# Performance work log

Measured on AMD Instinct MI355X. Metric: run time of the kernel, lower is better.

The kernel has to match this reference:

```python
import jax, jax.numpy as jnp
import numpy as np
from jax import lax

STRIDES = [4, 8, 16, 32, 64]
SIZES = [32.0, 64.0, 128.0, 256.0, 512.0]
RATIOS = [0.5, 1.0, 2.0]
IMG_H = IMG_W = 1024.0
NMS_T = 0.7
PRE = 1000      # PRE_NMS_TOPK_TEST
POST = 1000     # POST_NMS_TOPK_TEST
MIN_SIZE = 0.0
N = 2
FEAT = [(256, 256), (128, 128), (64, 64), (32, 32), (16, 16)]
SCALE_CLAMP = float(np.log(1000.0 / 16.0))


def make_anchors(H, W, stride, size):
    # detectron2 DefaultAnchorGenerator: area=size^2, w=sqrt(area/r), h=w*r; grid offsets = stride*arange
    r = np.array(RATIOS)
    ws = np.sqrt(size * size / r)
    hs = ws * r
    base = np.stack([-ws / 2, -hs / 2, ws / 2, hs / 2], axis=1)  # [A,4]
    sx = np.arange(W) * stride
    sy = np.arange(H) * stride
    yy, xx = np.meshgrid(sy, sx, indexing='ij')
    shifts = np.stack([xx, yy, xx, yy], axis=-1).reshape(-1, 1, 4)  # [H*W,1,4]
    return jnp.asarray((shifts + base[None]).reshape(-1, 4), jnp.float32)  # [H*W*A,4]


def conv2d(x, w, b, pad):
    y = lax.conv_general_dilated(x, w, (1, 1), [(pad, pad), (pad, pad)],
                                 dimension_numbers=('NCHW', 'OIHW', 'NCHW'))
    return y + b[None, :, None, None]


def apply_deltas(deltas, anchors):
    # Box2BoxTransform.apply_deltas with weights (1,1,1,1)
    w = anchors[..., 2] - anchors[..., 0]
    h = anchors[..., 3] - anchors[..., 1]
    cx = anchors[..., 0] + 0.5 * w
    cy = anchors[..., 1] + 0.5 * h
    dx, dy, dw, dh = deltas[..., 0], deltas[..., 1], deltas[..., 2], deltas[..., 3]
    dw = jnp.minimum(dw, SCALE_CLAMP)
    dh = jnp.minimum(dh, SCALE_CLAMP)
    pcx = dx * w + cx
    pcy = dy * h + cy
    pw = jnp.exp(dw) * w
    ph = jnp.exp(dh) * h
    return jnp.stack([pcx - 0.5 * pw, pcy - 0.5 * ph, pcx + 0.5 * pw, pcy + 0.5 * ph], axis=-1)


def pairwise_iou(b):
    area = (b[:, 2] - b[:, 0]) * (b[:, 3] - b[:, 1])
    lt = jnp.maximum(b[:, None, :2], b[None, :, :2])
    rb = jnp.minimum(b[:, None, 2:], b[None, :, 2:])
    wh = jnp.clip(rb - lt, 0.0)
    inter = wh[..., 0] * wh[..., 1]
    return inter / jnp.maximum(area[:, None] + area[None, :] - inter, 1e-9)


def nms_keep(boxes, valid):
    # boxes already sorted by score desc; sequential greedy NMS keep mask
    K = boxes.shape[0]
    M = pairwise_iou(boxes)
    idx = jnp.arange(K)

    def body(i, keep):
        sup = (M[i] > NMS_T) & (idx > i) & keep[i]
        return keep & (~sup)

    return lax.fori_loop(0, K, body, valid)


def rpn_forward(feats, conv_w, conv_b, obj_w, obj_b, delta_w, delta_b):
    all_boxes, all_scores = [], []
    lim = jnp.array([IMG_W, IMG_H, IMG_W, IMG_H], jnp.float32)
    for x, (H, W), stride, size in zip(feats, FEAT, STRIDES, SIZES):
        t = jax.nn.relu(conv2d(x, conv_w, conv_b, 1))
        logits = conv2d(t, obj_w, obj_b, 0)      # [N,A,H,W]
        deltas = conv2d(t, delta_w, delta_b, 0)  # [N,4A,H,W]
        A = logits.shape[1]
        logits = logits.transpose(0, 2, 3, 1).reshape(N, -1)                       # [N,H*W*A]
        deltas = deltas.reshape(N, A, 4, H, W).transpose(0, 3, 4, 1, 2).reshape(N, -1, 4)
        anchors = make_anchors(H, W, stride, size)
        props = apply_deltas(deltas, anchors[None])                                # [N,H*W*A,4]
        k = min(PRE, props.shape[1])
        scores, idx = lax.top_k(logits, k)                                         # [N,k]
        boxes = jnp.take_along_axis(props, idx[..., None], axis=1)                 # [N,k,4]
        boxes = jnp.clip(boxes, 0.0, lim)                                          # clip to image
        valid = ((boxes[..., 2] - boxes[..., 0]) > MIN_SIZE) & ((boxes[..., 3] - boxes[..., 1]) > MIN_SIZE)
        keep = lax.stop_gradient(jax.vmap(nms_keep)(boxes, valid))                 # NMS is no_grad in torch
        all_boxes.append(boxes)
        all_scores.append(jnp.where(keep, scores, -1e9))
    boxes = jnp.concatenate(all_boxes, axis=1)
    scores = jnp.concatenate(all_scores, axis=1)
    fs, fi = lax.top_k(scores, POST)                                               # final sort-by-score
    fb = jnp.take_along_axis(boxes, fi[..., None], axis=1)
    return fb, fs


def setup_inputs() -> dict:
    key = jax.random.key(0)
    ks = jax.random.split(key, 8)
    d = {}
    for i, (name, (H, W)) in enumerate(zip(['p2', 'p3', 'p4', 'p5', 'p6'], FEAT)):
        d[name] = jax.random.normal(ks[i], (N, 256, H, W), jnp.float32)
    d['conv_w'] = jax.random.normal(ks[5], (256, 256, 3, 3), jnp.float32) * 0.01
    d['conv_b'] = jnp.zeros((256,), jnp.float32)
    d['obj_w'] = jax.random.normal(ks[6], (3, 256, 1, 1), jnp.float32) * 0.01
    d['obj_b'] = jnp.zeros((3,), jnp.float32)
    d['delta_w'] = jax.random.normal(ks[7], (12, 256, 1, 1), jnp.float32) * 0.01
    d['delta_b'] = jnp.zeros((12,), jnp.float32)
    return d


def reference(p2, p3, p4, p5, p6, conv_w, conv_b, obj_w, obj_b, delta_w, delta_b):
    return rpn_forward([p2, p3, p4, p5, p6], conv_w, conv_b, obj_w, obj_b, delta_w, delta_b)
```

## Files before the change

kernel.cpp:

```cpp
#include <hip/hip_runtime.h>
#include <stdint.h>

#define DEVI __device__ __forceinline__

#define S_TOT 261888
#define NIMG  2
#define SCLD  4.135166556742356

__constant__ int    c_S[5]    = {196608, 49152, 12288, 3072, 768};
__constant__ int    c_loff[5] = {0, 196608, 245760, 258048, 261120};
__constant__ int    c_K[5]    = {1000, 1000, 1000, 1000, 768};
__constant__ int    c_Wl[5]   = {256, 128, 64, 32, 16};
__constant__ int    c_str[5]  = {4, 8, 16, 32, 64};
__constant__ double c_sz[5]   = {32.0, 64.0, 128.0, 256.0, 512.0};
__constant__ double c_rat[3]  = {0.5, 1.0, 2.0};
__constant__ int    c_boff[6] = {0, 512, 640, 672, 680, 682};
__constant__ int    c_Hl[5]   = {256, 128, 64, 32, 16};

DEVI unsigned key_of(float f) {
  unsigned u = __float_as_uint(f);
  return (u & 0x80000000u) ? ~u : (u | 0x80000000u);
}
DEVI float key_dec(unsigned k) {
  unsigned u = (k & 0x80000000u) ? (k & 0x7fffffffu) : ~k;
  return __uint_as_float(u);
}

__global__ void transpose_w(const float* __restrict__ w, float* __restrict__ wT2) {
  int k  = blockIdx.x;
  int co = threadIdx.x;
  int ci = k / 9, j = k - ci * 9;
  wT2[((size_t)(ci * 8 + (co >> 5))) * 288 + j * 32 + (co & 31)] = w[co * 2304 + k];
}

__global__ __launch_bounds__(512, 4) void conv_fused(
    const float* __restrict__ x0, const float* __restrict__ x1,
    const float* __restrict__ x2, const float* __restrict__ x3,
    const float* __restrict__ x4,
    const float* __restrict__ wT2,
    const float* __restrict__ cb, const float* __restrict__ ow,
    const float* __restrict__ ob, const float* __restrict__ dwt,
    const float* __restrict__ db, float* __restrict__ logits,
    float* __restrict__ deltas)
{
  __shared__ float lds[7680];
  const int tid = threadIdx.x;
  const int n = blockIdx.y;
  const int b = blockIdx.x;
  int l = 0;
#pragma unroll
  for (int q = 1; q < 5; ++q) if (b >= c_boff[q]) l = q;
  const int t = b - c_boff[l];
  const int H = c_Hl[l], W = H;
  const int tx = t & ((16 >> l) - 1), ty = t >> (4 - l);
  const int px0 = tx << 4, py0t = ty << 3;
  const int loff = c_loff[l];
  const float* xin = (l == 0) ? x0 : (l == 1) ? x1 : (l == 2) ? x2 : (l == 3) ? x3 : x4;
  xin += (size_t)n * 256 * H * W;

  const int lane = tid & 63, wv = tid >> 6;
  const int px = lane & 15, py = lane >> 4;
  const int cob = __builtin_amdgcn_readfirstlane(wv);
  const int co0 = cob << 5;

  float a0[32], a1[32];
#pragma unroll
  for (int i = 0; i < 32; ++i) { a0[i] = 0.f; a1[i] = 0.f; }

  for (int ch = 0; ch < 8; ++ch) {
    const int ci0 = ch << 5;
    __syncthreads();
    for (int tt = tid; tt < 32 * 180; tt += 512) {
      int ci = tt / 180, rem = tt % 180;
      int ry = rem / 18, rx = rem % 18;
      int gy = py0t + ry - 1, gx = px0 + rx - 1;
      float v = 0.f;
      if (gy >= 0 && gy < H && gx >= 0 && gx < W)
        v = xin[((size_t)(ci0 + ci) * H + gy) * W + gx];
      lds[tt] = v;
    }
    __syncthreads();
#pragma unroll 1
    for (int cc = 0; cc < 32; ++cc) {
      const int pb = cc * 180 + py * 18 + px;
      float pv0[9], pv1[9];
#pragma unroll
      for (int ky = 0; ky < 3; ++ky)
#pragma unroll
        for (int kx = 0; kx < 3; ++kx) {
          pv0[ky * 3 + kx] = lds[pb + ky * 18 + kx];
          pv1[ky * 3 + kx] = lds[pb + (ky + 4) * 18 + kx];
        }
      const float* wr = wT2 + ((size_t)((ci0 + cc) * 8 + cob)) * 288;
#pragma unroll
      for (int j = 0; j < 9; ++j) {
#pragma unroll
        for (int i = 0; i < 32; ++i) {
          const float wgt = wr[j * 32 + i];
          a0[i] = fmaf(wgt, pv0[j], a0[i]);
          a1[i] = fmaf(wgt, pv1[j], a1[i]);
        }
      }
    }
  }

#pragma unroll
  for (int h = 0; h < 2; ++h) {
    float part[15];
#pragma unroll
    for (int f = 0; f < 15; ++f) part[f] = 0.f;
#pragma unroll
    for (int i = 0; i < 32; ++i) {
      float v = (h ? a1[i] : a0[i]) + cb[co0 + i];
      float tv = fmaxf(v, 0.f);
#pragma unroll
      for (int f = 0; f < 3; ++f)  part[f]     = fmaf(tv, ow[f * 256 + co0 + i],  part[f]);
#pragma unroll
      for (int f = 0; f < 12; ++f) part[3 + f] = fmaf(tv, dwt[f * 256 + co0 + i], part[3 + f]);
    }
    __syncthreads();
#pragma unroll
    for (int f = 0; f < 15; ++f) lds[wv * 960 + f * 64 + lane] = part[f];
    __syncthreads();
    for (int tt = tid; tt < 960; tt += 512) {
      float s = 0.f;
#pragma unroll
      for (int w2 = 0; w2 < 8; ++w2) s += lds[w2 * 960 + tt];
      int f = tt >> 6, p = tt & 63;
      int gx = px0 + (p & 15), gy = py0t + (p >> 4) + 4 * h;
      int cell = gy * W + gx;
      if (f < 3) {
        logits[(size_t)n * S_TOT + loff + cell * 3 + f] = s + ob[f];
      } else {
        int chn = f - 3, a = chn >> 2, c = chn & 3;
        deltas[(((size_t)n * S_TOT + loff + cell * 3 + a) << 2) + c] = s + db[chn];
      }
    }
  }
}

__global__ __launch_bounds__(1024) void topk_kernel(
    const float* __restrict__ logits, const float* __restrict__ deltas,
    float* __restrict__ selscore, float* __restrict__ selbox,
    unsigned* __restrict__ selvalid)
{
  const int tid = threadIdx.x;
  const int nl = blockIdx.x, n = nl / 5, l = nl % 5;
  const int Sl = c_S[l], loff = c_loff[l], Kl = c_K[l], Wl = c_Wl[l], strl = c_str[l];
  const float* sc = logits + (size_t)n * S_TOT + loff;

  __shared__ unsigned hist[256];
  __shared__ unsigned sh_prefix, sh_need, s_base, s_cb;
  __shared__ unsigned waveTot[16], waveOff[16];
  __shared__ unsigned long long sortbuf[1024];

  unsigned prefix = 0, need = (unsigned)Kl;
  for (int p = 0; p < 4; ++p) {
    for (int i = tid; i < 256; i += 1024) hist[i] = 0;
    __syncthreads();
    const int shift = 24 - p * 8;
    for (int i = tid; i < Sl; i += 1024) {
      unsigned k = key_of(sc[i]);
      if (p == 0 || (k >> (shift + 8)) == prefix)
        atomicAdd(&hist[(k >> shift) & 255u], 1u);
    }
    __syncthreads();
    if (tid == 0) {
      unsigned cum = 0;
      for (int b = 255; b >= 0; --b) {
        unsigned c = hist[b];
        if (cum + c >= need) { sh_prefix = (prefix << 8) | (unsigned)b; sh_need = need - cum; break; }
        cum += c;
      }
    }
    __syncthreads();
    prefix = sh_prefix; need = sh_need;
    __syncthreads();
  }
  const unsigned Tkey = prefix;

  if (tid == 0) s_base = 0;
  __syncthreads();
  for (int pass = 0; pass < 2; ++pass) {
    for (int st = 0; st < Sl; st += 1024) {
      const int i = st + tid;
      bool flag = false; unsigned k = 0;
      if (i < Sl) {
        k = key_of(sc[i]);
        flag = (pass == 0) ? (k > Tkey) : (k == Tkey);
      }
      unsigned long long m = __ballot(flag);
      const int lane = tid & 63, w = tid >> 6;
      unsigned mypre = (unsigned)__popcll(m & ((1ull << lane) - 1ull));
      if (lane == 0) waveTot[w] = (unsigned)__popcll(m);
      __syncthreads();
      if (tid == 0) {
        unsigned ss = 0;
        for (int q = 0; q < 16; ++q) { waveOff[q] = ss; ss += waveTot[q]; }
        s_cb = s_base; s_base += ss;
      }
      __syncthreads();
      if (flag) {
        unsigned pos = s_cb + waveOff[w] + mypre;
        if (pos < (unsigned)Kl)
          sortbuf[pos] = (((unsigned long long)k) << 32) |
                         (unsigned long long)(0xFFFFFFFFu - (unsigned)i);
      }
      __syncthreads();
    }
  }
  if (tid >= Kl) sortbuf[tid] = (unsigned long long)(0xFFFFFFFFu - (unsigned)tid);
  __syncthreads();

  for (int k2 = 2; k2 <= 1024; k2 <<= 1) {
    for (int j = k2 >> 1; j > 0; j >>= 1) {
      const int i = tid, ixj = i ^ j;
      if (ixj > i) {
        unsigned long long a = sortbuf[i], b = sortbuf[ixj];
        const bool desc = (i & k2) == 0;
        if (desc ? (a < b) : (a > b)) { sortbuf[i] = b; sortbuf[ixj] = a; }
      }
      __syncthreads();
    }
  }

  const int r = tid;
  const int o = nl * 1024 + r;
  if (r < Kl) {
    unsigned long long v = sortbuf[r];
    unsigned k = (unsigned)(v >> 32);
    unsigned ai = 0xFFFFFFFFu - (unsigned)(v & 0xFFFFFFFFull);
    float score = key_dec(k);
    int cell = (int)(ai / 3u), a = (int)(ai % 3u);
    int xg = cell % Wl, yg = cell / Wl;
    double rr = c_rat[a], sz = c_sz[l];
    double wsd = sqrt(sz * sz / rr);
    double hw = 0.5 * wsd, hh = 0.5 * wsd * rr;
    double xs = (double)(xg * strl), ys = (double)(yg * strl);
    float a0 = (float)(xs - hw), a1 = (float)(ys - hh);
    float a2 = (float)(xs + hw), a3 = (float)(ys + hh);
    const float* dp = deltas + (((size_t)n * S_TOT + loff + ai) << 2);
    float dx = dp[0], dy = dp[1], dw_ = dp[2], dh_ = dp[3];
    float aw = a2 - a0, ah = a3 - a1;
    float cx = a0 + 0.5f * aw, cy = a1 + 0.5f * ah;
    dw_ = fminf(dw_, (float)SCLD); dh_ = fminf(dh_, (float)SCLD);
    float pcx = dx * aw + cx, pcy = dy * ah + cy;
    float pw = expf(dw_) * aw, ph = expf(dh_) * ah;
    float b0 = fminf(fmaxf(pcx - 0.5f * pw, 0.f), 1024.f);
    float b1 = fminf(fmaxf(pcy - 0.5f * ph, 0.f), 1024.f);
    float b2 = fminf(fmaxf(pcx + 0.5f * pw, 0.f), 1024.f);
    float b3 = fminf(fmaxf(pcy + 0.5f * ph, 0.f), 1024.f);
    unsigned valid = ((b2 - b0) > 0.f && (b3 - b1) > 0.f) ? 1u : 0u;
    selscore[o] = score;
    selbox[o * 4 + 0] = b0; selbox[o * 4 + 1] = b1;
    selbox[o * 4 + 2] = b2; selbox[o * 4 + 3] = b3;
    selvalid[o] = valid;
  } else {
    selscore[o] = -1e9f;
    selbox[o * 4 + 0] = 0.f; selbox[o * 4 + 1] = 0.f;
    selbox[o * 4 + 2] = 0.f; selbox[o * 4 + 3] = 0.f;
    selvalid[o] = 0u;
  }
}

__global__ __launch_bounds__(256) void nms_sup(
    const float* __restrict__ selbox, unsigned long long* __restrict__ sup)
{
  int gid = blockIdx.x * 256 + threadIdx.x;
  int w = gid & 15, i = (gid >> 4) & 1023, nl = gid >> 14;
  if (nl >= 10) return;
  int l = nl % 5, Kl = c_K[l];
  unsigned long long bits = 0;
  if (i < Kl) {
    const float* bi = selbox + (size_t)(nl * 1024 + i) * 4;
    float x0 = bi[0], y0 = bi[1], x1 = bi[2], y1 = bi[3];
    float ar = (x1 - x0) * (y1 - y0);
    int jlo = w * 64; if (jlo < i + 1) jlo = i + 1;
    int jhi = w * 64 + 64; if (jhi > Kl) jhi = Kl;
    for (int j = jlo; j < jhi; ++j) {
      const float* bj = selbox + (size_t)(nl * 1024 + j) * 4;
      float u0 = fmaxf(x0, bj[0]), v0 = fmaxf(y0, bj[1]);
      float u1 = fminf(x1, bj[2]), v1 = fminf(y1, bj[3]);
      float iw = fmaxf(u1 - u0, 0.f), ih = fmaxf(v1 - v0, 0.f);
      float inter = iw * ih;
      float aj = (bj[2] - bj[0]) * (bj[3] - bj[1]);
      float iou = inter / fmaxf(ar + aj - inter, 1e-9f);
      if (iou > 0.7f) bits |= 1ull << (j - w * 64);
    }
  }
  sup[(size_t)(nl * 1024 + i) * 16 + w] = bits;
}

__global__ __launch_bounds__(64) void nms_reduce(
    const unsigned* __restrict__ selvalid, const unsigned long long* __restrict__ sup,
    const float* __restrict__ selscore, float* __restrict__ scnms)
{
  const int nl = blockIdx.x, tid = threadIdx.x;
  const int l = nl % 5, Kl = c_K[l];
  unsigned long long keep = 0;
  if (tid < 16) {
    for (int t = 0; t < 64; ++t) {
      int r = tid * 64 + t;
      if (r < Kl && selvalid[nl * 1024 + r]) keep |= 1ull << t;
    }
  }
  const unsigned long long* srow = sup + (size_t)nl * 1024 * 16;
  unsigned long long rowA = (tid < 16) ? srow[(size_t)0 * 16 + tid] : 0;
  unsigned long long rowB = (tid < 16 && Kl > 1) ? srow[(size_t)1 * 16 + tid] : 0;
  for (int i = 0; i < Kl; i += 2) {
    unsigned long long kw = __shfl(keep, i >> 6);
    unsigned long long cur = rowA;
    rowA = (tid < 16 && i + 2 < Kl) ? srow[(size_t)(i + 2) * 16 + tid] : 0;
    if (((kw >> (i & 63)) & 1ull) && tid < 16) keep &= ~cur;
    kw = __shfl(keep, (i + 1) >> 6);
    cur = rowB;
    rowB = (tid < 16 && i + 3 < Kl) ? srow[(size_t)(i + 3) * 16 + tid] : 0;
    if (((kw >> ((i + 1) & 63)) & 1ull) && tid < 16) keep &= ~cur;
  }
  for (int r = tid; r < 1024; r += 64) {
    unsigned long long wv = __shfl(keep, r >> 6);
    bool kp = (r < Kl) && ((wv >> (r & 63)) & 1ull);
    scnms[nl * 1024 + r] = kp ? selscore[nl * 1024 + r] : -1e9f;
  }
}

DEVI float cand_score(const float* scnms, int n, int g) {
  int l = g / 1000;
  int r = g - l * 1000;
  return scnms[((n * 5 + l) << 10) + r];
}

__global__ __launch_bounds__(1024) void final_topk(
    const float* __restrict__ scnms, const float* __restrict__ selbox,
    float* __restrict__ out)
{
  const int tid = threadIdx.x;
  const int n = blockIdx.x;
  const int S = 4768;

  __shared__ unsigned hist[256];
  __shared__ unsigned sh_prefix, sh_need, s_base, s_cb;
  __shared__ unsigned waveTot[16], waveOff[16];
  __shared__ unsigned long long sortbuf[1024];

  unsigned prefix = 0, need = 1000;
  for (int p = 0; p < 4; ++p) {
    for (int i = tid; i < 256; i += 1024) hist[i] = 0;
    __syncthreads();
    const int shift = 24 - p * 8;
    for (int i = tid; i < S; i += 1024) {
      unsigned k = key_of(cand_score(scnms, n, i));
      if (p == 0 || (k >> (shift + 8)) == prefix)
        atomicAdd(&hist[(k >> shift) & 255u], 1u);
    }
    __syncthreads();
    if (tid == 0) {
      unsigned cum = 0;
      for (int b = 255; b >= 0; --b) {
        unsigned c = hist[b];
        if (cum + c >= need) { sh_prefix = (prefix << 8) | (unsigned)b; sh_need = need - cum; break; }
        cum += c;
      }
    }
    __syncthreads();
    prefix = sh_prefix; need = sh_need;
    __syncthreads();
  }
  const unsigned Tkey = prefix;

  if (tid == 0) s_base = 0;
  __syncthreads();
  for (int pass = 0; pass < 2; ++pass) {
    for (int st = 0; st < S; st += 1024) {
      const int i = st + tid;
      bool flag = false; unsigned k = 0;
      if (i < S) {
        k = key_of(cand_score(scnms, n, i));
        flag = (pass == 0) ? (k > Tkey) : (k == Tkey);
      }
      unsigned long long m = __ballot(flag);
      const int lane = tid & 63, w = tid >> 6;
      unsigned mypre = (unsigned)__popcll(m & ((1ull << lane) - 1ull));
      if (lane == 0) waveTot[w] = (unsigned)__popcll(m);
      __syncthreads();
      if (tid == 0) {
        unsigned ss = 0;
        for (int q = 0; q < 16; ++q) { waveOff[q] = ss; ss += waveTot[q]; }
        s_cb = s_base; s_base += ss;
      }
      __syncthreads();
      if (flag) {
        unsigned pos = s_cb + waveOff[w] + mypre;
        if (pos < 1000u)
          sortbuf[pos] = (((unsigned long long)k) << 32) |
                         (unsigned long long)(0xFFFFFFFFu - (unsigned)i);
      }
      __syncthreads();
    }
  }
  if (tid >= 1000) sortbuf[tid] = (unsigned long long)(0xFFFFFFFFu - (unsigned)tid);
  __syncthreads();

  for (int k2 = 2; k2 <= 1024; k2 <<= 1) {
    for (int j = k2 >> 1; j > 0; j >>= 1) {
      const int i = tid, ixj = i ^ j;
      if (ixj > i) {
        unsigned long long a = sortbuf[i], b = sortbuf[ixj];
        const bool desc = (i & k2) == 0;
        if (desc ? (a < b) : (a > b)) { sortbuf[i] = b; sortbuf[ixj] = a; }
      }
      __syncthreads();
    }
  }

  if (tid < 1000) {
    unsigned long long v = sortbuf[tid];
    unsigned k = (unsigned)(v >> 32);
    int g = (int)(0xFFFFFFFFu - (unsigned)(v & 0xFFFFFFFFull));
    int l = g / 1000, r = g - l * 1000;
    const float* b = selbox + ((size_t)((n * 5 + l) * 1024 + r)) * 4;
    size_t ob_ = ((size_t)n * 1000 + tid) * 4;
    out[ob_ + 0] = b[0]; out[ob_ + 1] = b[1];
    out[ob_ + 2] = b[2]; out[ob_ + 3] = b[3];
    out[8000 + n * 1000 + tid] = key_dec(k);
  }
}

extern "C" void kernel_launch(void* const* d_in, const int* in_sizes, int n_in,
                              void* d_out, int out_size, void* d_ws, size_t ws_size,
                              hipStream_t stream)
{
  const float* feats[5];
  for (int i = 0; i < 5; ++i) feats[i] = (const float*)d_in[i];
  const float* conv_w  = (const float*)d_in[5];
  const float* conv_b  = (const float*)d_in[6];
  const float* obj_w   = (const float*)d_in[7];
  const float* obj_b   = (const float*)d_in[8];
  const float* delta_w = (const float*)d_in[9];
  const float* delta_b = (const float*)d_in[10];

  char* wsp = (char*)d_ws;
  float* wT2      = (float*)wsp;  wsp += (size_t)2304 * 256 * 4;
  float* logits   = (float*)wsp;  wsp += (size_t)NIMG * S_TOT * 4;
  float* deltas   = (float*)wsp;  wsp += (size_t)NIMG * S_TOT * 16;
  float* selscore = (float*)wsp;  wsp += (size_t)10 * 1024 * 4;
  float* selbox   = (float*)wsp;  wsp += (size_t)10 * 1024 * 16;
  unsigned* selvalid = (unsigned*)wsp; wsp += (size_t)10 * 1024 * 4;
  float* scnms    = (float*)wsp;  wsp += (size_t)10 * 1024 * 4;
  unsigned long long* sup = (unsigned long long*)wsp;
  wsp += (size_t)10 * 1024 * 16 * 8;

  transpose_w<<<dim3(2304), dim3(256), 0, stream>>>(conv_w, wT2);

  conv_fused<<<dim3(682, NIMG), dim3(512), 0, stream>>>(
      feats[0], feats[1], feats[2], feats[3], feats[4],
      wT2, conv_b, obj_w, obj_b, delta_w, delta_b, logits, deltas);

  topk_kernel<<<dim3(10), dim3(1024), 0, stream>>>(logits, deltas,
                                                   selscore, selbox, selvalid);
  nms_sup<<<dim3(640), dim3(256), 0, stream>>>(selbox, sup);
  nms_reduce<<<dim3(10), dim3(64), 0, stream>>>(selvalid, sup, selscore, scnms);
  final_topk<<<dim3(NIMG), dim3(1024), 0, stream>>>(scnms, selbox, (float*)d_out);
}
```

Measured before the change: 3.504 ms.

## Retile conv to 16x16 pixel tiles with 16-channel groups in two passes

The fused 3x3 conv now covers a 16x16 pixel tile per block instead of 16x8, which halves the block count. Each wave computes 16 output channels for 4 pixel rows, and output channels are covered in two passes. Each wave-uniform weight is now reused across four pixels instead of two, cutting weight loads per FMA. The price is that the input halo is staged into LDS twice (once per pass) and partial head results are written to global memory and read back in the second pass. There are also fewer blocks to fill the GPU.

```diff
diff --git a/kernel.cpp b/kernel.cpp
--- a/kernel.cpp
+++ b/kernel.cpp
@@ -14,7 +14,7 @@
 __constant__ int    c_str[5]  = {4, 8, 16, 32, 64};
 __constant__ double c_sz[5]   = {32.0, 64.0, 128.0, 256.0, 512.0};
 __constant__ double c_rat[3]  = {0.5, 1.0, 2.0};
-__constant__ int    c_boff[6] = {0, 512, 640, 672, 680, 682};
+__constant__ int    c_boff[6] = {0, 256, 320, 336, 340, 341};
 __constant__ int    c_Hl[5]   = {256, 128, 64, 32, 16};
 
 DEVI unsigned key_of(float f) {
@@ -30,7 +30,7 @@
   int k  = blockIdx.x;
   int co = threadIdx.x;
   int ci = k / 9, j = k - ci * 9;
-  wT2[((size_t)(ci * 8 + (co >> 5))) * 288 + j * 32 + (co & 31)] = w[co * 2304 + k];
+  wT2[((size_t)(ci * 16 + (co >> 4))) * 144 + j * 16 + (co & 15)] = w[co * 2304 + k];
 }
 
 __global__ __launch_bounds__(512, 4) void conv_fused(
@@ -52,88 +52,101 @@
   for (int q = 1; q < 5; ++q) if (b >= c_boff[q]) l = q;
   const int t = b - c_boff[l];
   const int H = c_Hl[l], W = H;
-  const int tx = t & ((16 >> l) - 1), ty = t >> (4 - l);
-  const int px0 = tx << 4, py0t = ty << 3;
+  const int tilesx = 16 >> l;
+  const int tx = t & (tilesx - 1), ty = t >> (4 - l);
+  const int px0 = tx << 4, py0 = ty << 4;
   const int loff = c_loff[l];
   const float* xin = (l == 0) ? x0 : (l == 1) ? x1 : (l == 2) ? x2 : (l == 3) ? x3 : x4;
   xin += (size_t)n * 256 * H * W;
 
   const int lane = tid & 63, wv = tid >> 6;
-  const int px = lane & 15, py = lane >> 4;
-  const int cob = __builtin_amdgcn_readfirstlane(wv);
-  const int co0 = cob << 5;
-
-  float a0[32], a1[32];
-#pragma unroll
-  for (int i = 0; i < 32; ++i) { a0[i] = 0.f; a1[i] = 0.f; }
-
-  for (int ch = 0; ch < 8; ++ch) {
-    const int ci0 = ch << 5;
-    __syncthreads();
-    for (int tt = tid; tt < 32 * 180; tt += 512) {
-      int ci = tt / 180, rem = tt % 180;
-      int ry = rem / 18, rx = rem % 18;
-      int gy = py0t + ry - 1, gx = px0 + rx - 1;
-      float v = 0.f;
-      if (gy >= 0 && gy < H && gx >= 0 && gx < W)
-        v = xin[((size_t)(ci0 + ci) * H + gy) * W + gx];
-      lds[tt] = v;
-    }
-    __syncthreads();
+  const int px = lane & 15, p = lane >> 4;
+
+  for (int pass = 0; pass < 2; ++pass) {
+    const int g = (pass << 3) + __builtin_amdgcn_readfirstlane(wv);
+    const int co0 = g << 4;
+
+    float acc[4][16];
+#pragma unroll
+    for (int k = 0; k < 4; ++k)
+#pragma unroll
+      for (int i = 0; i < 16; ++i) acc[k][i] = 0.f;
+
+    for (int ch = 0; ch < 16; ++ch) {
+      const int ci0 = ch << 4;
+      __syncthreads();
+      for (int tt = tid; tt < 16 * 324; tt += 512) {
+        int ci = tt / 324, rem = tt - ci * 324;
+        int ry = rem / 18, rx = rem - ry * 18;
+        int gy = py0 + ry - 1, gx = px0 + rx - 1;
+        float v = 0.f;
+        if (gy >= 0 && gy < H && gx >= 0 && gx < W)
+          v = xin[((size_t)(ci0 + ci) * H + gy) * W + gx];
+        lds[tt] = v;
+      }
+      __syncthreads();
 #pragma unroll 1
-    for (int cc = 0; cc < 32; ++cc) {
-      const int pb = cc * 180 + py * 18 + px;
-      float pv0[9], pv1[9];
-#pragma unroll
-      for (int ky = 0; ky < 3; ++ky)
-#pragma unroll
-        for (int kx = 0; kx < 3; ++kx) {
-          pv0[ky * 3 + kx] = lds[pb + ky * 18 + kx];
-          pv1[ky * 3 + kx] = lds[pb + (ky + 4) * 18 + kx];
+      for (int cc = 0; cc < 16; ++cc) {
+        const int pb = cc * 324 + p * 18 + px;
+        const float* wr = wT2 + ((size_t)((ci0 + cc) * 16 + g)) * 144;
+#pragma unroll
+        for (int ky = 0; ky < 3; ++ky) {
+          float pvk[4][3];
+#pragma unroll
+          for (int k = 0; k < 4; ++k)
+#pragma unroll
+            for (int kx = 0; kx < 3; ++kx)
+              pvk[k][kx] = lds[pb + ((k << 2) + ky) * 18 + kx];
+#pragma unroll
+          for (int kx = 0; kx < 3; ++kx) {
+#pragma unroll
+            for (int i = 0; i < 16; ++i) {
+              const float wgt = wr[(ky * 3 + kx) * 16 + i];
+#pragma unroll
+              for (int k = 0; k < 4; ++k)
+                acc[k][i] = fmaf(wgt, pvk[k][kx], acc[k][i]);
+            }
+          }
         }
-      const float* wr = wT2 + ((size_t)((ci0 + cc) * 8 + cob)) * 288;
-#pragma unroll
-      for (int j = 0; j < 9; ++j) {
-#pragma unroll
-        for (int i = 0; i < 32; ++i) {
-          const float wgt = wr[j * 32 + i];
-          a0[i] = fmaf(wgt, pv0[j], a0[i]);
-          a1[i] = fmaf(wgt, pv1[j], a1[i]);
+      }
+    }
+
+#pragma unroll 1
+    for (int k = 0; k < 4; ++k) {
+      float part[15];
+#pragma unroll
+      for (int f = 0; f < 15; ++f) part[f] = 0.f;
+#pragma unroll
+      for (int i = 0; i < 16; ++i) {
+        float tv = fmaxf(acc[k][i] + cb[co0 + i], 0.f);
+#pragma unroll
+        for (int f = 0; f < 3; ++f)  part[f]     = fmaf(tv, ow[f * 256 + co0 + i],  part[f]);
+#pragma unroll
+        for (int f = 0; f < 12; ++f) part[3 + f] = fmaf(tv, dwt[f * 256 + co0 + i], part[3 + f]);
+      }
+      __syncthreads();
+#pragma unroll
+      for (int f = 0; f < 15; ++f) lds[wv * 960 + f * 64 + lane] = part[f];
+      __syncthreads();
+      for (int tt = tid; tt < 960; tt += 512) {
+        int f = tt >> 6, pp = tt & 63;
+        int gx = px0 + (pp & 15), gy = py0 + (pp >> 4) + (k << 2);
+        int cell = gy * W + gx;
+        size_t adr;
+        float bias;
+        if (f < 3) {
+          adr = (size_t)n * S_TOT + loff + cell * 3 + f;
+          bias = ob[f];
+        } else {
+          int chn = f - 3, a = chn >> 2, c = chn & 3;
+          adr = (((size_t)n * S_TOT + loff + cell * 3 + a) << 2) + c;
+          bias = db[chn];
         }
-      }
-    }
-  }
-
-#pragma unroll
-  for (int h = 0; h < 2; ++h) {
-    float part[15];
-#pragma unroll
-    for (int f = 0; f < 15; ++f) part[f] = 0.f;
-#pragma unroll
-    for (int i = 0; i < 32; ++i) {
-      float v = (h ? a1[i] : a0[i]) + cb[co0 + i];
-      float tv = fmaxf(v, 0.f);
-#pragma unroll
-      for (int f = 0; f < 3; ++f)  part[f]     = fmaf(tv, ow[f * 256 + co0 + i],  part[f]);
-#pragma unroll
-      for (int f = 0; f < 12; ++f) part[3 + f] = fmaf(tv, dwt[f * 256 + co0 + i], part[3 + f]);
-    }
-    __syncthreads();
-#pragma unroll
-    for (int f = 0; f < 15; ++f) lds[wv * 960 + f * 64 + lane] = part[f];
-    __syncthreads();
-    for (int tt = tid; tt < 960; tt += 512) {
-      float s = 0.f;
-#pragma unroll
-      for (int w2 = 0; w2 < 8; ++w2) s += lds[w2 * 960 + tt];
-      int f = tt >> 6, p = tt & 63;
-      int gx = px0 + (p & 15), gy = py0t + (p >> 4) + 4 * h;
-      int cell = gy * W + gx;
-      if (f < 3) {
-        logits[(size_t)n * S_TOT + loff + cell * 3 + f] = s + ob[f];
-      } else {
-        int chn = f - 3, a = chn >> 2, c = chn & 3;
-        deltas[(((size_t)n * S_TOT + loff + cell * 3 + a) << 2) + c] = s + db[chn];
+        float* dst = (f < 3) ? logits : deltas;
+        float s = (pass == 0) ? 0.f : dst[adr];
+#pragma unroll
+        for (int w2 = 0; w2 < 8; ++w2) s += lds[w2 * 960 + tt];
+        dst[adr] = (pass == 0) ? s : (s + bias);
       }
     }
   }
@@ -452,7 +465,7 @@
 
   transpose_w<<<dim3(2304), dim3(256), 0, stream>>>(conv_w, wT2);
 
-  conv_fused<<<dim3(682, NIMG), dim3(512), 0, stream>>>(
+  conv_fused<<<dim3(341, NIMG), dim3(512), 0, stream>>>(
       feats[0], feats[1], feats[2], feats[3], feats[4],
       wT2, conv_b, obj_w, obj_b, delta_w, delta_b, logits, deltas);
 
```

Measured after the change: 3.736 ms. +6.6%, slower.

## Stage conv weights in LDS per 8-channel chunk with float4 reads

Applied to the files above, without the earlier changes.

Weights are re-laid out into 8-input-channel chunks and copied cooperatively into shared memory with float4 loads each iteration. The 3x3 conv inner loop then reads them from LDS as float4 instead of from global or scalar memory, and the input tile shrinks to 8 channels per stage. The intent is to cut repeated global weight fetches, at the cost of about 79KB of LDS per block, which lowers occupancy and means four times as many barriers.

```diff
diff --git a/kernel.cpp b/kernel.cpp
--- a/kernel.cpp
+++ b/kernel.cpp
@@ -26,24 +26,27 @@
   return __uint_as_float(u);
 }
 
-__global__ void transpose_w(const float* __restrict__ w, float* __restrict__ wT2) {
+__global__ void transpose_w(const float* __restrict__ w, float* __restrict__ wT3) {
   int k  = blockIdx.x;
   int co = threadIdx.x;
   int ci = k / 9, j = k - ci * 9;
-  wT2[((size_t)(ci * 8 + (co >> 5))) * 288 + j * 32 + (co & 31)] = w[co * 2304 + k];
+  int chunk = ci >> 3, cc = ci & 7;
+  int g = co >> 5, i = co & 31;
+  wT3[(size_t)chunk * 18432 + cc * 2304 + g * 288 + j * 32 + i] = w[co * 2304 + k];
 }
 
 __global__ __launch_bounds__(512, 4) void conv_fused(
     const float* __restrict__ x0, const float* __restrict__ x1,
     const float* __restrict__ x2, const float* __restrict__ x3,
     const float* __restrict__ x4,
-    const float* __restrict__ wT2,
+    const float* __restrict__ wT3,
     const float* __restrict__ cb, const float* __restrict__ ow,
     const float* __restrict__ ob, const float* __restrict__ dwt,
     const float* __restrict__ db, float* __restrict__ logits,
     float* __restrict__ deltas)
 {
-  __shared__ float lds[7680];
+  __shared__ float lds[19872];
+  float* const wlds = lds + 1440;
   const int tid = threadIdx.x;
   const int n = blockIdx.y;
   const int b = blockIdx.x;
@@ -52,58 +55,71 @@
   for (int q = 1; q < 5; ++q) if (b >= c_boff[q]) l = q;
   const int t = b - c_boff[l];
   const int H = c_Hl[l], W = H;
-  const int tx = t & ((16 >> l) - 1), ty = t >> (4 - l);
-  const int px0 = tx << 4, py0t = ty << 3;
+  const int tilesx = 16 >> l;
+  const int tx = t & (tilesx - 1), ty = t >> (4 - l);
+  const int px0 = tx << 4, py0 = ty << 3;
   const int loff = c_loff[l];
   const float* xin = (l == 0) ? x0 : (l == 1) ? x1 : (l == 2) ? x2 : (l == 3) ? x3 : x4;
   xin += (size_t)n * 256 * H * W;
 
   const int lane = tid & 63, wv = tid >> 6;
-  const int px = lane & 15, py = lane >> 4;
-  const int cob = __builtin_amdgcn_readfirstlane(wv);
-  const int co0 = cob << 5;
+  const int px = lane & 15, p = lane >> 4;
 
   float a0[32], a1[32];
 #pragma unroll
   for (int i = 0; i < 32; ++i) { a0[i] = 0.f; a1[i] = 0.f; }
 
-  for (int ch = 0; ch < 8; ++ch) {
-    const int ci0 = ch << 5;
-    __syncthreads();
-    for (int tt = tid; tt < 32 * 180; tt += 512) {
-      int ci = tt / 180, rem = tt % 180;
-      int ry = rem / 18, rx = rem % 18;
-      int gy = py0t + ry - 1, gx = px0 + rx - 1;
+  for (int ch = 0; ch < 32; ++ch) {
+    const int ci0 = ch << 3;
+    __syncthreads();
+    for (int tt = tid; tt < 1440; tt += 512) {
+      int ci = tt / 180, rem = tt - ci * 180;
+      int ry = rem / 18, rx = rem - ry * 18;
+      int gy = py0 + ry - 1, gx = px0 + rx - 1;
       float v = 0.f;
       if (gy >= 0 && gy < H && gx >= 0 && gx < W)
         v = xin[((size_t)(ci0 + ci) * H + gy) * W + gx];
       lds[tt] = v;
     }
+    {
+      const float4* wg = (const float4*)(wT3 + (size_t)ch * 18432);
+      float4* wl = (float4*)wlds;
+      for (int tt = tid; tt < 4608; tt += 512) wl[tt] = wg[tt];
+    }
     __syncthreads();
 #pragma unroll 1
-    for (int cc = 0; cc < 32; ++cc) {
-      const int pb = cc * 180 + py * 18 + px;
-      float pv0[9], pv1[9];
-#pragma unroll
-      for (int ky = 0; ky < 3; ++ky)
+    for (int cc = 0; cc < 8; ++cc) {
+      const float* wr = wlds + cc * 2304 + wv * 288;
+      const int pb = cc * 180 + p * 18 + px;
+#pragma unroll 1
+      for (int ky = 0; ky < 3; ++ky) {
+        const int rb = pb + ky * 18;
+        const float q00 = lds[rb + 0],  q01 = lds[rb + 1],  q02 = lds[rb + 2];
+        const float q10 = lds[rb + 72], q11 = lds[rb + 73], q12 = lds[rb + 74];
+        const float* wk = wr + ky * 96;
 #pragma unroll
         for (int kx = 0; kx < 3; ++kx) {
-          pv0[ky * 3 + kx] = lds[pb + ky * 18 + kx];
-          pv1[ky * 3 + kx] = lds[pb + (ky + 4) * 18 + kx];
+          const float pv0 = (kx == 0) ? q00 : (kx == 1) ? q01 : q02;
+          const float pv1 = (kx == 0) ? q10 : (kx == 1) ? q11 : q12;
+          const float* wt = wk + kx * 32;
+#pragma unroll
+          for (int iq = 0; iq < 8; ++iq) {
+            const float4 wq = *(const float4*)(wt + (iq << 2));
+            a0[iq * 4 + 0] = fmaf(wq.x, pv0, a0[iq * 4 + 0]);
+            a0[iq * 4 + 1] = fmaf(wq.y, pv0, a0[iq * 4 + 1]);
+            a0[iq * 4 + 2] = fmaf(wq.z, pv0, a0[iq * 4 + 2]);
+            a0[iq * 4 + 3] = fmaf(wq.w, pv0, a0[iq * 4 + 3]);
+            a1[iq * 4 + 0] = fmaf(wq.x, pv1, a1[iq * 4 + 0]);
+            a1[iq * 4 + 1] = fmaf(wq.y, pv1, a1[iq * 4 + 1]);
+            a1[iq * 4 + 2] = fmaf(wq.z, pv1, a1[iq * 4 + 2]);
+            a1[iq * 4 + 3] = fmaf(wq.w, pv1, a1[iq * 4 + 3]);
+          }
         }
-      const float* wr = wT2 + ((size_t)((ci0 + cc) * 8 + cob)) * 288;
-#pragma unroll
-      for (int j = 0; j < 9; ++j) {
-#pragma unroll
-        for (int i = 0; i < 32; ++i) {
-          const float wgt = wr[j * 32 + i];
-          a0[i] = fmaf(wgt, pv0[j], a0[i]);
-          a1[i] = fmaf(wgt, pv1[j], a1[i]);
-        }
-      }
-    }
-  }
-
+      }
+    }
+  }
+
+  const int co0 = __builtin_amdgcn_readfirstlane(wv << 5);
 #pragma unroll
   for (int h = 0; h < 2; ++h) {
     float part[15];
@@ -126,8 +142,8 @@
       float s = 0.f;
 #pragma unroll
       for (int w2 = 0; w2 < 8; ++w2) s += lds[w2 * 960 + tt];
-      int f = tt >> 6, p = tt & 63;
-      int gx = px0 + (p & 15), gy = py0t + (p >> 4) + 4 * h;
+      int f = tt >> 6, pp = tt & 63;
+      int gx = px0 + (pp & 15), gy = py0 + (pp >> 4) + 4 * h;
       int cell = gy * W + gx;
       if (f < 3) {
         logits[(size_t)n * S_TOT + loff + cell * 3 + f] = s + ob[f];
@@ -440,7 +456,7 @@
   const float* delta_b = (const float*)d_in[10];
 
   char* wsp = (char*)d_ws;
-  float* wT2      = (float*)wsp;  wsp += (size_t)2304 * 256 * 4;
+  float* wT3      = (float*)wsp;  wsp += (size_t)2304 * 256 * 4;
   float* logits   = (float*)wsp;  wsp += (size_t)NIMG * S_TOT * 4;
   float* deltas   = (float*)wsp;  wsp += (size_t)NIMG * S_TOT * 16;
   float* selscore = (float*)wsp;  wsp += (size_t)10 * 1024 * 4;
@@ -450,11 +466,11 @@
   unsigned long long* sup = (unsigned long long*)wsp;
   wsp += (size_t)10 * 1024 * 16 * 8;
 
-  transpose_w<<<dim3(2304), dim3(256), 0, stream>>>(conv_w, wT2);
+  transpose_w<<<dim3(2304), dim3(256), 0, stream>>>(conv_w, wT3);
 
   conv_fused<<<dim3(682, NIMG), dim3(512), 0, stream>>>(
       feats[0], feats[1], feats[2], feats[3], feats[4],
-      wT2, conv_b, obj_w, obj_b, delta_w, delta_b, logits, deltas);
+      wT3, conv_b, obj_w, obj_b, delta_w, delta_b, logits, deltas);
 
   topk_kernel<<<dim3(10), dim3(1024), 0, stream>>>(logits, deltas,
                                                    selscore, selbox, selvalid);
```

Result: slower. 3.695 ms (+5.5%).
